# Kernel tuning notes

Hardware: AMD Instinct MI355X
Metric: run time of the kernel (lower is better)

The kernel has to match this reference:

```python
import jax, jax.numpy as jnp
import numpy as np
import math

V, P, D, L, H = 50257, 1024, 768, 12, 12
HD = D // H
DFF = 4 * D
B, S = 2, 1024
EPS = 1e-5


def setup_inputs() -> dict:
    key = jax.random.key(0)
    ks = jax.random.split(key, 8)
    sc = 0.02
    return {
        "input_ids": jax.random.randint(ks[0], (B, S), 0, V),
        "wte": jax.random.normal(ks[1], (V, D), jnp.float32) * sc,
        "wpe": jax.random.normal(ks[2], (P, D), jnp.float32) * sc,
        "ln1_g": jnp.ones((L, D), jnp.float32),
        "ln1_b": jnp.zeros((L, D), jnp.float32),
        "qkv_w": jax.random.normal(ks[3], (L, 3 * D, D), jnp.float32) * sc,
        "qkv_b": jnp.zeros((L, 3 * D), jnp.float32),
        "proj_w": jax.random.normal(ks[4], (L, D, D), jnp.float32) * sc,
        "proj_b": jnp.zeros((L, D), jnp.float32),
        "ln2_g": jnp.ones((L, D), jnp.float32),
        "ln2_b": jnp.zeros((L, D), jnp.float32),
        "fc_w": jax.random.normal(ks[5], (L, DFF, D), jnp.float32) * sc,
        "fc_b": jnp.zeros((L, DFF), jnp.float32),
        "cproj_w": jax.random.normal(ks[6], (L, D, DFF), jnp.float32) * sc,
        "cproj_b": jnp.zeros((L, D), jnp.float32),
        "lnf_g": jnp.ones((D,), jnp.float32),
        "lnf_b": jnp.zeros((D,), jnp.float32),
    }


def layer_norm(x, g, b):
    mu = jnp.mean(x, axis=-1, keepdims=True)
    var = jnp.mean(jnp.square(x - mu), axis=-1, keepdims=True)
    return (x - mu) * jax.lax.rsqrt(var + EPS) * g + b


def _forward(input_ids, wte, wpe, ln1_g, ln1_b, qkv_w, qkv_b, proj_w, proj_b,
             ln2_g, ln2_b, fc_w, fc_b, cproj_w, cproj_b, lnf_g, lnf_b):
    s = input_ids.shape[1]
    h = wte[input_ids] + wpe[jnp.arange(s)][None, :, :]  # [B,S,D]
    causal = jnp.tril(jnp.ones((s, s), bool))  # [S,S]
    neg_inf = jnp.finfo(h.dtype).min

    def step(x, p):
        l1g, l1b, qw, qb, pw, pb, l2g, l2b, fw, fb, cw, cb = p
        hn = layer_norm(x, l1g, l1b)
        qkv = hn @ qw.T + qb  # [B,S,3D]
        q, k, v = jnp.split(qkv, 3, axis=-1)
        q = q.reshape(B, s, H, HD).transpose(0, 2, 1, 3)  # [B,H,S,hd]
        k = k.reshape(B, s, H, HD).transpose(0, 2, 1, 3)
        v = v.reshape(B, s, H, HD).transpose(0, 2, 1, 3)
        scores = jnp.einsum("bhqd,bhkd->bhqk", q, k) / math.sqrt(HD)
        scores = jnp.where(causal[None, None], scores, neg_inf)
        attn = jax.nn.softmax(scores, axis=-1)
        o = jnp.einsum("bhqk,bhkd->bhqd", attn, v)
        o = o.transpose(0, 2, 1, 3).reshape(B, s, D)
        x = x + (o @ pw.T + pb)
        hn2 = layer_norm(x, l2g, l2b)
        m = jax.nn.gelu(hn2 @ fw.T + fb, approximate=False)
        x = x + (m @ cw.T + cb)
        return x, None

    params = (ln1_g, ln1_b, qkv_w, qkv_b, proj_w, proj_b,
              ln2_g, ln2_b, fc_w, fc_b, cproj_w, cproj_b)
    h, _ = jax.lax.scan(step, h, params)
    h = layer_norm(h, lnf_g, lnf_b)
    logits = h @ wte.T  # tied lm_head, [B,S,V]
    return logits


def reference(input_ids, wte, wpe, ln1_g, ln1_b, qkv_w, qkv_b, proj_w, proj_b,
              ln2_g, ln2_b, fc_w, fc_b, cproj_w, cproj_b, lnf_g, lnf_b):
    return _forward(input_ids, wte, wpe, ln1_g, ln1_b, qkv_w, qkv_b, proj_w,
                    proj_b, ln2_g, ln2_b, fc_w, fc_b, cproj_w, cproj_b,
                    lnf_g, lnf_b)
```

## Files before the change

### kernel.cpp

```cpp
#include <hip/hip_runtime.h>

#define BB 2
#define SS 1024
#define DM 768
#define NH 12
#define HDIM 64
#define NL 12
#define DFFN 3072
#define VOC 50257
#define ROWS (BB * SS)
#define MT (ROWS / 128)

typedef __attribute__((ext_vector_type(4))) float f32x4;
typedef __attribute__((ext_vector_type(8))) short short8;
typedef __attribute__((ext_vector_type(4))) short short4v;
typedef unsigned short ushort;

__device__ __forceinline__ ushort f2bf(float f) {
  union { float f; unsigned int u; } x; x.f = f;
  unsigned int u = x.u;
  unsigned int r = (u + 0x7FFFu + ((u >> 16) & 1u)) >> 16;
  return (ushort)r;
}

__global__ __launch_bounds__(256) void embed_k(const int* __restrict__ ids,
    const float* __restrict__ wte, const float* __restrict__ wpe,
    float* __restrict__ h) {
  const int row = blockIdx.x;
  const int s = row & (SS - 1);
  const int tid = threadIdx.x;
  const int id = ids[row];
  const size_t wbase = (size_t)id * DM;
  const size_t pbase = (size_t)s * DM;
  const size_t obase = (size_t)row * DM;
  h[obase + tid]       = wte[wbase + tid]       + wpe[pbase + tid];
  h[obase + tid + 256] = wte[wbase + tid + 256] + wpe[pbase + tid + 256];
  h[obase + tid + 512] = wte[wbase + tid + 512] + wpe[pbase + tid + 512];
}

__global__ __launch_bounds__(256) void f2b_k(const float* __restrict__ in,
                                             ushort* __restrict__ out, int n4) {
  for (int i = blockIdx.x * 256 + threadIdx.x; i < n4; i += gridDim.x * 256) {
    f32x4 v = ((const f32x4*)in)[i];
    short4v s;
    s[0] = f2bf(v[0]); s[1] = f2bf(v[1]); s[2] = f2bf(v[2]); s[3] = f2bf(v[3]);
    ((short4v*)out)[i] = s;
  }
}

template <int OB>
__global__ __launch_bounds__(256) void layernorm_t(const float* __restrict__ x,
    const float* __restrict__ g, const float* __restrict__ b, void* __restrict__ y) {
  const int tid = threadIdx.x;
  const size_t base = (size_t)blockIdx.x * DM;
  float v0 = x[base + tid], v1 = x[base + tid + 256], v2 = x[base + tid + 512];
  __shared__ float red[256];
  red[tid] = v0 + v1 + v2;
  __syncthreads();
  for (int off = 128; off > 0; off >>= 1) {
    if (tid < off) red[tid] += red[tid + off];
    __syncthreads();
  }
  float mu = red[0] * (1.0f / DM);
  __syncthreads();
  float d0 = v0 - mu, d1 = v1 - mu, d2 = v2 - mu;
  red[tid] = d0 * d0 + d1 * d1 + d2 * d2;
  __syncthreads();
  for (int off = 128; off > 0; off >>= 1) {
    if (tid < off) red[tid] += red[tid + off];
    __syncthreads();
  }
  float rstd = rsqrtf(red[0] * (1.0f / DM) + 1e-5f);
  float o0 = d0 * rstd * g[tid]       + b[tid];
  float o1 = d1 * rstd * g[tid + 256] + b[tid + 256];
  float o2 = d2 * rstd * g[tid + 512] + b[tid + 512];
  if (OB) {
    ushort* yo = (ushort*)y;
    yo[base + tid] = f2bf(o0); yo[base + tid + 256] = f2bf(o1);
    yo[base + tid + 512] = f2bf(o2);
  } else {
    float* yo = (float*)y;
    yo[base + tid] = o0; yo[base + tid + 256] = o1; yo[base + tid + 512] = o2;
  }
}

template <int ROUNDS>
__device__ __forceinline__ void stage_sw(const ushort* __restrict__ g, int ldg,
                                         ushort* lds, int wave, int lane,
                                         int rowmax) {
#pragma unroll
  for (int r = 0; r < ROUNDS; r++) {
    const int chunk = (r * 4 + wave) * 64 + lane;
    const int nrow = chunk >> 3;
    const int cs = (chunk & 7) ^ (nrow & 7);
    const int row = nrow > rowmax ? rowmax : nrow;
    const ushort* ga = g + (size_t)row * ldg + cs * 8;
    ushort* la = lds + (r * 4 + wave) * 512;
    __builtin_amdgcn_global_load_lds(
        (const __attribute__((address_space(1))) unsigned int*)ga,
        (__attribute__((address_space(3))) unsigned int*)la, 16, 0, 0);
  }
}

template <int EPI, int OUTBF, int NF>
__global__ __launch_bounds__(256) void gemm_bf(const ushort* __restrict__ A,
    const ushort* __restrict__ Bw, const float* __restrict__ bias,
    const float* __restrict__ res, void* __restrict__ Cout, int N, int K) {
  __shared__ __align__(16) ushort AsL[2][128 * 64];
  __shared__ __align__(16) ushort BsL[2][NF * 32 * 64];
  const int tid = threadIdx.x;
  const int lane = tid & 63;
  const int wave = tid >> 6;
  const int la = lane & 15;
  const int hi = lane >> 4;
  const int swz = (la & 7) << 3;

  const int nwg = gridDim.x;
  int bid = blockIdx.x;
  {
    const int q = nwg >> 3, r = nwg & 7;
    const int xcd = bid & 7, idx = bid >> 3;
    bid = (xcd < r ? xcd * (q + 1) : r * (q + 1) + (xcd - r) * q) + idx;
  }
  const int m0 = (bid % MT) * 128;
  const int n0 = (bid / MT) * (NF * 32);

  const int wr = (wave >> 1) * 64;
  const int wc = (wave & 1) * (NF * 16);
  const int brmax = min(N - n0 - 1, NF * 32 - 1);

  f32x4 acc[4][NF];
#pragma unroll
  for (int i = 0; i < 4; i++)
#pragma unroll
    for (int j = 0; j < NF; j++) acc[i][j] = (f32x4){0.f, 0.f, 0.f, 0.f};

  const ushort* Ag = A + (size_t)m0 * K;
  const ushort* Bg = Bw + (size_t)n0 * K;

  const int nt = K >> 6;
  const int s0 = (bid % MT) % nt;

  stage_sw<4>(Ag + s0 * 64, K, AsL[0], wave, lane, 127);
  stage_sw<NF>(Bg + s0 * 64, K, BsL[0], wave, lane, brmax);

  int cur = 0;
  for (int t = 0; t < nt; t++) {
    if (t + 1 < nt) {
      int sn = t + 1 + s0; if (sn >= nt) sn -= nt;
      stage_sw<4>(Ag + sn * 64, K, AsL[cur ^ 1], wave, lane, 127);
      stage_sw<NF>(Bg + sn * 64, K, BsL[cur ^ 1], wave, lane, brmax);
      asm volatile("s_waitcnt vmcnt(%0)" :: "i"(4 + NF) : "memory");
    } else {
      asm volatile("s_waitcnt vmcnt(0)" ::: "memory");
    }
    __builtin_amdgcn_s_barrier();
    __builtin_amdgcn_sched_barrier(0);

    const ushort* Ab = AsL[cur] + (wr + la) * 64;
    const ushort* Bb = BsL[cur] + (wc + la) * 64;
    __builtin_amdgcn_s_setprio(1);
#pragma unroll
    for (int ks = 0; ks < 2; ks++) {
      const int co = (ks * 32 + hi * 8) ^ swz;
      short8 a[4], b[NF];
#pragma unroll
      for (int mi = 0; mi < 4; mi++)
        a[mi] = *(const short8*)(Ab + mi * 1024 + co);
#pragma unroll
      for (int ni = 0; ni < NF; ni++)
        b[ni] = *(const short8*)(Bb + ni * 1024 + co);
#pragma unroll
      for (int mi = 0; mi < 4; mi++)
#pragma unroll
        for (int ni = 0; ni < NF; ni++)
          acc[mi][ni] = __builtin_amdgcn_mfma_f32_16x16x32_bf16(
              a[mi], b[ni], acc[mi][ni], 0, 0, 0);
    }
    __builtin_amdgcn_s_setprio(0);
    __builtin_amdgcn_sched_barrier(0);
    __builtin_amdgcn_s_barrier();
    __builtin_amdgcn_sched_barrier(0);
    cur ^= 1;
  }

#pragma unroll
  for (int mi = 0; mi < 4; mi++)
#pragma unroll
    for (int ni = 0; ni < NF; ni++) {
      const int col = n0 + wc + ni * 16 + la;
      if (col < N) {
#pragma unroll
        for (int j = 0; j < 4; j++) {
          const int row = m0 + wr + mi * 16 + 4 * hi + j;
          float x = acc[mi][ni][j];
          if (EPI >= 1) x += bias[col];
          const size_t idx = (size_t)row * N + col;
          if (EPI == 2) x += res[idx];
          if (EPI == 3) x = 0.5f * x * (1.0f + erff(x * 0.70710678118f));
          if (OUTBF) ((ushort*)Cout)[idx] = f2bf(x);
          else       ((float*)Cout)[idx] = x;
        }
      }
    }
}

template <int EPI, int OUTBF, int MR>
__global__ __launch_bounds__(256) void gemm_p3(const ushort* __restrict__ A,
    const ushort* __restrict__ Bw, const float* __restrict__ bias,
    const float* __restrict__ res, void* __restrict__ Cout, int N, int K) {
  constexpr int MROWS = MR * 32;
  constexpr int MTILES = ROWS / MROWS;
  constexpr int ASZ = MROWS * 64;
  constexpr int BSZ = 64 * 64;
  __shared__ __align__(16) ushort smem[3 * ASZ + 3 * BSZ];
  ushort* As = smem;
  ushort* Bs = smem + 3 * ASZ;

  const int tid = threadIdx.x;
  const int lane = tid & 63;
  const int wave = tid >> 6;
  const int la = lane & 15;
  const int hi = lane >> 4;
  const int swz = (la & 7) << 3;

  const int nwg = gridDim.x;
  int bid = blockIdx.x;
  {
    const int q = nwg >> 3, r = nwg & 7;
    const int xcd = bid & 7, idx = bid >> 3;
    bid = (xcd < r ? xcd * (q + 1) : r * (q + 1) + (xcd - r) * q) + idx;
  }
  const int m0 = (bid % MTILES) * MROWS;
  const int n0 = (bid / MTILES) * 64;

  const int wr = (wave >> 1) * (MROWS / 2);
  const int wc = (wave & 1) * 32;

  f32x4 acc[MR][2];
#pragma unroll
  for (int i = 0; i < MR; i++)
#pragma unroll
    for (int j = 0; j < 2; j++) acc[i][j] = (f32x4){0.f, 0.f, 0.f, 0.f};

  const ushort* Ag = A + (size_t)m0 * K;
  const ushort* Bg = Bw + (size_t)n0 * K;
  const int nt = K >> 6;
  const int s0 = (bid % MTILES) % nt;

  {
    int s1 = s0 + 1; if (s1 >= nt) s1 -= nt;
    stage_sw<MR>(Ag + s0 * 64, K, As, wave, lane, MROWS - 1);
    stage_sw<2>(Bg + s0 * 64, K, Bs, wave, lane, 63);
    stage_sw<MR>(Ag + s1 * 64, K, As + ASZ, wave, lane, MROWS - 1);
    stage_sw<2>(Bg + s1 * 64, K, Bs + BSZ, wave, lane, 63);
  }

  for (int t = 0; t < nt; t++) {
    if (t + 1 < nt) {
      asm volatile("s_waitcnt vmcnt(%0)" :: "i"(MR + 2) : "memory");
    } else {
      asm volatile("s_waitcnt vmcnt(0)" ::: "memory");
    }
    __builtin_amdgcn_s_barrier();
    __builtin_amdgcn_sched_barrier(0);

    const ushort* Ab = As + (t % 3) * ASZ + (wr + la) * 64;
    const ushort* Bb = Bs + (t % 3) * BSZ + (wc + la) * 64;
    __builtin_amdgcn_s_setprio(1);
#pragma unroll
    for (int ks = 0; ks < 2; ks++) {
      const int co = (ks * 32 + hi * 8) ^ swz;
      short8 a[MR], b[2];
#pragma unroll
      for (int mi = 0; mi < MR; mi++)
        a[mi] = *(const short8*)(Ab + mi * 1024 + co);
#pragma unroll
      for (int ni = 0; ni < 2; ni++)
        b[ni] = *(const short8*)(Bb + ni * 1024 + co);
#pragma unroll
      for (int mi = 0; mi < MR; mi++)
#pragma unroll
        for (int ni = 0; ni < 2; ni++)
          acc[mi][ni] = __builtin_amdgcn_mfma_f32_16x16x32_bf16(
              a[mi], b[ni], acc[mi][ni], 0, 0, 0);
    }
    __builtin_amdgcn_s_setprio(0);
    __builtin_amdgcn_sched_barrier(0);
    __builtin_amdgcn_s_barrier();
    __builtin_amdgcn_sched_barrier(0);
    if (t + 2 < nt) {
      int sn = t + 2 + s0; if (sn >= nt) sn -= nt;
      stage_sw<MR>(Ag + sn * 64, K, As + ((t + 2) % 3) * ASZ, wave, lane, MROWS - 1);
      stage_sw<2>(Bg + sn * 64, K, Bs + ((t + 2) % 3) * BSZ, wave, lane, 63);
    }
  }

  if (OUTBF) {
    ushort* L = smem;
#pragma unroll
    for (int mi = 0; mi < MR; mi++)
#pragma unroll
      for (int ni = 0; ni < 2; ni++)
#pragma unroll
        for (int j = 0; j < 4; j++) {
          const int row = wr + mi * 16 + 4 * hi + j;
          const int col = wc + ni * 16 + la;
          float x = acc[mi][ni][j];
          if (EPI >= 1) x += bias[n0 + col];
          if (EPI == 3) x = 0.5f * x * (1.0f + erff(x * 0.70710678118f));
          L[row * 72 + col] = f2bf(x);
        }
    __syncthreads();
    ushort* Co = (ushort*)Cout;
    constexpr int ITERS = MROWS * 64 / 8 / 256;
#pragma unroll
    for (int it = 0; it < ITERS; it++) {
      const int idx8 = it * 256 + tid;
      const int row = idx8 >> 3, c8 = idx8 & 7;
      short8 v = *(const short8*)&L[row * 72 + c8 * 8];
      *(short8*)&Co[(size_t)(m0 + row) * N + n0 + c8 * 8] = v;
    }
  } else {
    float* L = (float*)smem;
#pragma unroll
    for (int mi = 0; mi < MR; mi++)
#pragma unroll
      for (int ni = 0; ni < 2; ni++)
#pragma unroll
        for (int j = 0; j < 4; j++) {
          const int row = wr + mi * 16 + 4 * hi + j;
          const int col = wc + ni * 16 + la;
          float x = acc[mi][ni][j];
          if (EPI >= 1) x += bias[n0 + col];
          if (EPI == 3) x = 0.5f * x * (1.0f + erff(x * 0.70710678118f));
          L[row * 68 + col] = x;
        }
    __syncthreads();
    f32x4* Co = (f32x4*)Cout;
    const f32x4* R4 = (const f32x4*)res;
    constexpr int ITERS = MROWS * 64 / 4 / 256;
#pragma unroll
    for (int it = 0; it < ITERS; it++) {
      const int idx4 = it * 256 + tid;
      const int row = idx4 >> 4, c4 = idx4 & 15;
      f32x4 v = *(const f32x4*)&L[row * 68 + c4 * 4];
      const size_t o4 = ((size_t)(m0 + row) * N + n0) / 4 + c4;
      if (EPI == 2) v += R4[o4];
      Co[o4] = v;
    }
  }
}

__global__ __launch_bounds__(256) void attn_bf(const ushort* __restrict__ qkv,
                                               ushort* __restrict__ o) {
  const int tid = threadIdx.x;
  const int lane = tid & 63;
  const int wave = tid >> 6;
  const int hi = lane >> 4;
  const int la = lane & 15;
  const int q0 = blockIdx.x * 64;
  const int bh = blockIdx.y;
  const int bb = bh / NH;
  const int hh = bh % NH;
  const size_t rstride = 3 * DM;
  const ushort* base = qkv + (size_t)bb * SS * rstride;

  __shared__ ushort Ks[64][72];
  __shared__ ushort Vt[64][72];
  __shared__ ushort Pb[4][16][72];

  short8 qf[2];
  {
    const int qrow = q0 + wave * 16 + la;
    const ushort* qp = base + (size_t)qrow * rstride + hh * HDIM + 8 * hi;
    qf[0] = *(const short8*)qp;
    qf[1] = *(const short8*)(qp + 32);
  }

  f32x4 accO[4] = {};
  float m_[4], l_[4];
#pragma unroll
  for (int j = 0; j < 4; j++) { m_[j] = -1e30f; l_[j] = 0.f; }

  const int nt = q0 / 64 + 1;
  for (int kt = 0; kt < nt; kt++) {
    __syncthreads();
    {
      const int r = tid >> 2;
      const int c = (tid & 3) * 16;
      const ushort* kp = base + (size_t)(kt * 64 + r) * rstride + DM + hh * HDIM + c;
      const ushort* vp = kp + DM;
      *(short8*)&Ks[r][c]     = *(const short8*)kp;
      *(short8*)&Ks[r][c + 8] = *(const short8*)(kp + 8);
      short8 v0 = *(const short8*)vp;
      short8 v1 = *(const short8*)(vp + 8);
#pragma unroll
      for (int i = 0; i < 8; i++) {
        Vt[c + i][r]     = (ushort)v0[i];
        Vt[c + 8 + i][r] = (ushort)v1[i];
      }
    }
    __syncthreads();

    f32x4 s[4] = {};
#pragma unroll
    for (int f = 0; f < 4; f++) {
#pragma unroll
      for (int kk = 0; kk < 2; kk++) {
        short8 kf = *(const short8*)&Ks[f * 16 + la][kk * 32 + 8 * hi];
        s[f] = __builtin_amdgcn_mfma_f32_16x16x32_bf16(qf[kk], kf, s[f], 0, 0, 0);
      }
#pragma unroll
      for (int j = 0; j < 4; j++) s[f][j] *= 0.125f;
    }

    if (kt == nt - 1) {
      const int qr = wave * 16 + 4 * hi;
#pragma unroll
      for (int f = 0; f < 4; f++) {
        const int kcol = f * 16 + la;
#pragma unroll
        for (int j = 0; j < 4; j++)
          if (kcol > qr + j) s[f][j] = -1e30f;
      }
    }

#pragma unroll
    for (int j = 0; j < 4; j++) {
      float rm = fmaxf(fmaxf(s[0][j], s[1][j]), fmaxf(s[2][j], s[3][j]));
      rm = fmaxf(rm, __shfl_xor(rm, 1));
      rm = fmaxf(rm, __shfl_xor(rm, 2));
      rm = fmaxf(rm, __shfl_xor(rm, 4));
      rm = fmaxf(rm, __shfl_xor(rm, 8));
      const float mnew = fmaxf(m_[j], rm);
      const float alpha = expf(m_[j] - mnew);
      float rs = 0.f;
#pragma unroll
      for (int f = 0; f < 4; f++) {
        const float p = expf(s[f][j] - mnew);
        s[f][j] = p;
        rs += p;
      }
      rs += __shfl_xor(rs, 1);
      rs += __shfl_xor(rs, 2);
      rs += __shfl_xor(rs, 4);
      rs += __shfl_xor(rs, 8);
      l_[j] = l_[j] * alpha + rs;
      m_[j] = mnew;
#pragma unroll
      for (int f = 0; f < 4; f++) accO[f][j] *= alpha;
    }

#pragma unroll
    for (int f = 0; f < 4; f++)
#pragma unroll
      for (int j = 0; j < 4; j++)
        Pb[wave][4 * hi + j][f * 16 + la] = f2bf(s[f][j]);

    short8 pf0 = *(const short8*)&Pb[wave][la][8 * hi];
    short8 pf1 = *(const short8*)&Pb[wave][la][32 + 8 * hi];
#pragma unroll
    for (int f = 0; f < 4; f++) {
      short8 vf0 = *(const short8*)&Vt[f * 16 + la][8 * hi];
      short8 vf1 = *(const short8*)&Vt[f * 16 + la][32 + 8 * hi];
      accO[f] = __builtin_amdgcn_mfma_f32_16x16x32_bf16(pf0, vf0, accO[f], 0, 0, 0);
      accO[f] = __builtin_amdgcn_mfma_f32_16x16x32_bf16(pf1, vf1, accO[f], 0, 0, 0);
    }
  }

  ushort* op = o + (size_t)(bb * SS + q0 + wave * 16) * DM + hh * HDIM;
#pragma unroll
  for (int j = 0; j < 4; j++) {
    const float inv = 1.0f / l_[j];
    const int qr = 4 * hi + j;
#pragma unroll
    for (int f = 0; f < 4; f++)
      op[(size_t)qr * DM + f * 16 + la] = f2bf(accO[f][j] * inv);
  }
}

template <int EPI>
__global__ __launch_bounds__(256) void gemm_nt(const float* __restrict__ A,
    const float* __restrict__ Bw, const float* __restrict__ bias,
    const float* __restrict__ res, float* __restrict__ C, int N, int K) {
  __shared__ ushort As[64][40];
  __shared__ ushort Bs[64][40];
  const int tid = threadIdx.x;
  const int m0 = blockIdx.y * 64;
  const int n0 = blockIdx.x * 64;
  const int lane = tid & 63;
  const int wave = tid >> 6;
  const int wr = (wave >> 1) * 32;
  const int wc = (wave & 1) * 32;
  const int lr = lane & 15;
  const int lk = (lane >> 4) * 8;
  const int sr = tid >> 2;
  const int sc = (tid & 3) * 8;
  f32x4 acc[2][2] = {};
  for (int kk = 0; kk < K; kk += 32) {
    {
      const float* p = A + (size_t)(m0 + sr) * K + kk + sc;
      f32x4 v0 = *(const f32x4*)p;
      f32x4 v1 = *(const f32x4*)(p + 4);
      short8 sv;
      for (int i = 0; i < 4; i++) { sv[i] = f2bf(v0[i]); sv[4 + i] = f2bf(v1[i]); }
      *(short8*)&As[sr][sc] = sv;
    }
    {
      const int gr = n0 + sr;
      short8 sv = {};
      if (gr < N) {
        const float* p = Bw + (size_t)gr * K + kk + sc;
        f32x4 v0 = *(const f32x4*)p;
        f32x4 v1 = *(const f32x4*)(p + 4);
        for (int i = 0; i < 4; i++) { sv[i] = f2bf(v0[i]); sv[4 + i] = f2bf(v1[i]); }
      }
      *(short8*)&Bs[sr][sc] = sv;
    }
    __syncthreads();
    short8 a0 = *(const short8*)&As[wr + lr][lk];
    short8 a1 = *(const short8*)&As[wr + 16 + lr][lk];
    short8 b0 = *(const short8*)&Bs[wc + lr][lk];
    short8 b1 = *(const short8*)&Bs[wc + 16 + lr][lk];
    acc[0][0] = __builtin_amdgcn_mfma_f32_16x16x32_bf16(a0, b0, acc[0][0], 0, 0, 0);
    acc[0][1] = __builtin_amdgcn_mfma_f32_16x16x32_bf16(a0, b1, acc[0][1], 0, 0, 0);
    acc[1][0] = __builtin_amdgcn_mfma_f32_16x16x32_bf16(a1, b0, acc[1][0], 0, 0, 0);
    acc[1][1] = __builtin_amdgcn_mfma_f32_16x16x32_bf16(a1, b1, acc[1][1], 0, 0, 0);
    __syncthreads();
  }
  const int orow = (lane >> 4) * 4;
  for (int mi = 0; mi < 2; mi++)
    for (int ni = 0; ni < 2; ni++) {
      const int col = n0 + wc + ni * 16 + lr;
      if (col >= N) continue;
      for (int j = 0; j < 4; j++) {
        const int row = m0 + wr + mi * 16 + orow + j;
        float x = acc[mi][ni][j];
        if (EPI >= 1) x += bias[col];
        const size_t idx = (size_t)row * N + col;
        if (EPI == 2) x += res[idx];
        if (EPI == 3) x = 0.5f * x * (1.0f + erff(x * 0.70710678118f));
        C[idx] = x;
      }
    }
}

__global__ __launch_bounds__(256) void attn_f32(const float* __restrict__ qkv,
                                                float* __restrict__ o) {
  const int tid = threadIdx.x;
  const int lane = tid & 63;
  const int wave = tid >> 6;
  const int hi = lane >> 4;
  const int la = lane & 15;
  const int q0 = blockIdx.x * 64;
  const int bh = blockIdx.y;
  const int bb = bh / NH;
  const int hh = bh % NH;
  const size_t rstride = 3 * DM;
  const float* base = qkv + (size_t)bb * SS * rstride;
  __shared__ ushort Ks[64][72];
  __shared__ ushort Vt[64][72];
  __shared__ ushort Pb[4][16][72];
  short8 qf[2];
  {
    const int qrow = q0 + wave * 16 + la;
    const float* qp = base + (size_t)qrow * rstride + hh * HDIM + 8 * hi;
    for (int kk = 0; kk < 2; kk++) {
      f32x4 v0 = *(const f32x4*)(qp + 32 * kk);
      f32x4 v1 = *(const f32x4*)(qp + 32 * kk + 4);
      short8 sv;
      for (int i = 0; i < 4; i++) {
        sv[i] = f2bf(v0[i] * 0.125f); sv[4 + i] = f2bf(v1[i] * 0.125f);
      }
      qf[kk] = sv;
    }
  }
  f32x4 accO[4] = {};
  float m_[4], l_[4];
  for (int j = 0; j < 4; j++) { m_[j] = -1e30f; l_[j] = 0.f; }
  const int nt = q0 / 64 + 1;
  for (int kt = 0; kt < nt; kt++) {
    __syncthreads();
    {
      const int r = tid >> 2;
      const int c = (tid & 3) * 16;
      const float* kp = base + (size_t)(kt * 64 + r) * rstride + DM + hh * HDIM + c;
      const float* vp = kp + DM;
      f32x4 k0 = *(const f32x4*)kp, k1 = *(const f32x4*)(kp + 4);
      f32x4 k2 = *(const f32x4*)(kp + 8), k3 = *(const f32x4*)(kp + 12);
      short8 s0, s1;
      for (int i = 0; i < 4; i++) {
        s0[i] = f2bf(k0[i]); s0[4 + i] = f2bf(k1[i]);
        s1[i] = f2bf(k2[i]); s1[4 + i] = f2bf(k3[i]);
      }
      *(short8*)&Ks[r][c] = s0;
      *(short8*)&Ks[r][c + 8] = s1;
      f32x4 v0 = *(const f32x4*)vp, v1 = *(const f32x4*)(vp + 4);
      f32x4 v2 = *(const f32x4*)(vp + 8), v3 = *(const f32x4*)(vp + 12);
      for (int i = 0; i < 4; i++) {
        Vt[c + i][r] = f2bf(v0[i]); Vt[c + 4 + i][r] = f2bf(v1[i]);
        Vt[c + 8 + i][r] = f2bf(v2[i]); Vt[c + 12 + i][r] = f2bf(v3[i]);
      }
    }
    __syncthreads();
    f32x4 s[4] = {};
    for (int f = 0; f < 4; f++)
      for (int kk = 0; kk < 2; kk++) {
        short8 kf = *(const short8*)&Ks[f * 16 + la][kk * 32 + 8 * hi];
        s[f] = __builtin_amdgcn_mfma_f32_16x16x32_bf16(qf[kk], kf, s[f], 0, 0, 0);
      }
    if (kt == nt - 1) {
      const int qr = wave * 16 + 4 * hi;
      for (int f = 0; f < 4; f++) {
        const int kcol = f * 16 + la;
        for (int j = 0; j < 4; j++)
          if (kcol > qr + j) s[f][j] = -1e30f;
      }
    }
    for (int j = 0; j < 4; j++) {
      float rm = fmaxf(fmaxf(s[0][j], s[1][j]), fmaxf(s[2][j], s[3][j]));
      rm = fmaxf(rm, __shfl_xor(rm, 1));
      rm = fmaxf(rm, __shfl_xor(rm, 2));
      rm = fmaxf(rm, __shfl_xor(rm, 4));
      rm = fmaxf(rm, __shfl_xor(rm, 8));
      const float mnew = fmaxf(m_[j], rm);
      const float alpha = expf(m_[j] - mnew);
      float rs = 0.f;
      for (int f = 0; f < 4; f++) {
        const float p = expf(s[f][j] - mnew);
        s[f][j] = p; rs += p;
      }
      rs += __shfl_xor(rs, 1);
      rs += __shfl_xor(rs, 2);
      rs += __shfl_xor(rs, 4);
      rs += __shfl_xor(rs, 8);
      l_[j] = l_[j] * alpha + rs;
      m_[j] = mnew;
      for (int f = 0; f < 4; f++) accO[f][j] *= alpha;
    }
    for (int f = 0; f < 4; f++)
      for (int j = 0; j < 4; j++)
        Pb[wave][4 * hi + j][f * 16 + la] = f2bf(s[f][j]);
    short8 pf0 = *(const short8*)&Pb[wave][la][8 * hi];
    short8 pf1 = *(const short8*)&Pb[wave][la][32 + 8 * hi];
    for (int f = 0; f < 4; f++) {
      short8 vf0 = *(const short8*)&Vt[f * 16 + la][8 * hi];
      short8 vf1 = *(const short8*)&Vt[f * 16 + la][32 + 8 * hi];
      accO[f] = __builtin_amdgcn_mfma_f32_16x16x32_bf16(pf0, vf0, accO[f], 0, 0, 0);
      accO[f] = __builtin_amdgcn_mfma_f32_16x16x32_bf16(pf1, vf1, accO[f], 0, 0, 0);
    }
  }
  float* op = o + (size_t)(bb * SS + q0 + wave * 16) * DM + hh * HDIM;
  for (int j = 0; j < 4; j++) {
    const float inv = 1.0f / l_[j];
    const int qr = 4 * hi + j;
    for (int f = 0; f < 4; f++)
      op[(size_t)qr * DM + f * 16 + la] = accO[f][j] * inv;
  }
}

extern "C" void kernel_launch(void* const* d_in, const int* in_sizes, int n_in,
                              void* d_out, int out_size, void* d_ws,
                              size_t ws_size, hipStream_t stream) {
  const int*   ids     = (const int*)d_in[0];
  const float* wte     = (const float*)d_in[1];
  const float* wpe     = (const float*)d_in[2];
  const float* ln1_g   = (const float*)d_in[3];
  const float* ln1_b   = (const float*)d_in[4];
  const float* qkv_w   = (const float*)d_in[5];
  const float* qkv_b   = (const float*)d_in[6];
  const float* proj_w  = (const float*)d_in[7];
  const float* proj_b  = (const float*)d_in[8];
  const float* ln2_g   = (const float*)d_in[9];
  const float* ln2_b   = (const float*)d_in[10];
  const float* fc_w    = (const float*)d_in[11];
  const float* fc_b    = (const float*)d_in[12];
  const float* cproj_w = (const float*)d_in[13];
  const float* cproj_b = (const float*)d_in[14];
  const float* lnf_g   = (const float*)d_in[15];
  const float* lnf_b   = (const float*)d_in[16];
  float* out = (float*)d_out;

  const size_t sz_h    = (size_t)ROWS * DM * 4;
  const size_t sz_hn   = (size_t)ROWS * DM * 2;
  const size_t sz_qkv  = (size_t)ROWS * 3 * DM * 2;
  const size_t sz_ob   = (size_t)ROWS * DM * 2;
  const size_t sz_mb   = (size_t)ROWS * DFFN * 2;
  const size_t sz_wq   = (size_t)NL * 3 * DM * DM * 2;
  const size_t sz_wp   = (size_t)NL * DM * DM * 2;
  const size_t sz_wf   = (size_t)NL * DFFN * DM * 2;
  const size_t sz_wc   = (size_t)NL * DM * DFFN * 2;
  const size_t sz_wt   = (size_t)VOC * DM * 2;
  const size_t NEED = sz_h + sz_hn + sz_qkv + sz_ob + sz_mb +
                      sz_wq + sz_wp + sz_wf + sz_wc + sz_wt;

  if (ws_size >= NEED) {
    char* p = (char*)d_ws;
    float*  h    = (float*)p;  p += sz_h;
    ushort* hn   = (ushort*)p; p += sz_hn;
    ushort* qkvb = (ushort*)p; p += sz_qkv;
    ushort* ob   = (ushort*)p; p += sz_ob;
    ushort* mb   = (ushort*)p; p += sz_mb;
    ushort* wq   = (ushort*)p; p += sz_wq;
    ushort* wp   = (ushort*)p; p += sz_wp;
    ushort* wf   = (ushort*)p; p += sz_wf;
    ushort* wc   = (ushort*)p; p += sz_wc;
    ushort* wt   = (ushort*)p; p += sz_wt;

    f2b_k<<<2048, 256, 0, stream>>>(qkv_w,   wq, NL * 3 * DM * DM / 4);
    f2b_k<<<1024, 256, 0, stream>>>(proj_w,  wp, NL * DM * DM / 4);
    f2b_k<<<2048, 256, 0, stream>>>(fc_w,    wf, NL * DFFN * DM / 4);
    f2b_k<<<2048, 256, 0, stream>>>(cproj_w, wc, NL * DM * DFFN / 4);
    f2b_k<<<2048, 256, 0, stream>>>(wte,     wt, VOC * DM / 4);

    embed_k<<<ROWS, 256, 0, stream>>>(ids, wte, wpe, h);

    for (int l = 0; l < NL; l++) {
      layernorm_t<1><<<ROWS, 256, 0, stream>>>(h, ln1_g + l * DM, ln1_b + l * DM, hn);
      gemm_p3<1, 1, 4><<<MT * (3 * DM / 64), 256, 0, stream>>>(
          hn, wq + (size_t)l * 3 * DM * DM, qkv_b + (size_t)l * 3 * DM,
          nullptr, qkvb, 3 * DM, DM);
      attn_bf<<<dim3(SS / 64, BB * NH), 256, 0, stream>>>(qkvb, ob);
      gemm_p3<2, 0, 2><<<(ROWS / 64) * (DM / 64), 256, 0, stream>>>(
          ob, wp + (size_t)l * DM * DM, proj_b + (size_t)l * DM, h, h, DM, DM);
      layernorm_t<1><<<ROWS, 256, 0, stream>>>(h, ln2_g + l * DM, ln2_b + l * DM, hn);
      gemm_p3<3, 1, 4><<<MT * (DFFN / 64), 256, 0, stream>>>(
          hn, wf + (size_t)l * DFFN * DM, fc_b + (size_t)l * DFFN,
          nullptr, mb, DFFN, DM);
      gemm_p3<2, 0, 2><<<(ROWS / 64) * (DM / 64), 256, 0, stream>>>(
          mb, wc + (size_t)l * DM * DFFN, cproj_b + (size_t)l * DM, h, h,
          DM, DFFN);
    }

    layernorm_t<1><<<ROWS, 256, 0, stream>>>(h, lnf_g, lnf_b, hn);
    gemm_bf<0, 0, 4><<<MT * ((VOC + 127) / 128), 256, 0, stream>>>(
        hn, wt, nullptr, nullptr, out, VOC, DM);
  } else {
    float* ws = (float*)d_ws;
    float* h   = ws;
    float* hn  = h + (size_t)ROWS * DM;
    float* qkv = hn + (size_t)ROWS * DM;
    float* ob  = qkv + (size_t)ROWS * 3 * DM;
    float* mb  = ob + (size_t)ROWS * DM;

    embed_k<<<ROWS, 256, 0, stream>>>(ids, wte, wpe, h);
    for (int l = 0; l < NL; l++) {
      layernorm_t<0><<<ROWS, 256, 0, stream>>>(h, ln1_g + l * DM, ln1_b + l * DM, hn);
      gemm_nt<1><<<dim3(3 * DM / 64, ROWS / 64), 256, 0, stream>>>(
          hn, qkv_w + (size_t)l * 3 * DM * DM, qkv_b + (size_t)l * 3 * DM,
          nullptr, qkv, 3 * DM, DM);
      attn_f32<<<dim3(SS / 64, BB * NH), 256, 0, stream>>>(qkv, ob);
      gemm_nt<2><<<dim3(DM / 64, ROWS / 64), 256, 0, stream>>>(
          ob, proj_w + (size_t)l * DM * DM, proj_b + (size_t)l * DM, h, h, DM, DM);
      layernorm_t<0><<<ROWS, 256, 0, stream>>>(h, ln2_g + l * DM, ln2_b + l * DM, hn);
      gemm_nt<3><<<dim3(DFFN / 64, ROWS / 64), 256, 0, stream>>>(
          hn, fc_w + (size_t)l * DFFN * DM, fc_b + (size_t)l * DFFN,
          nullptr, mb, DFFN, DM);
      gemm_nt<2><<<dim3(DM / 64, ROWS / 64), 256, 0, stream>>>(
          mb, cproj_w + (size_t)l * DM * DFFN, cproj_b + (size_t)l * DM, h, h,
          DM, DFFN);
    }
    layernorm_t<0><<<ROWS, 256, 0, stream>>>(h, lnf_g, lnf_b, hn);
    gemm_nt<0><<<dim3((VOC + 63) / 64, ROWS / 64), 256, 0, stream>>>(
        hn, wte, nullptr, nullptr, out, VOC, DM);
  }
}
```

Before: 2.073 ms.

## Replace GEMM kernels with 64x64 deep-pipelined tiles and prefetch attention K/V

Swaps the layer GEMMs for a 64x64-tile kernel with a 5-buffer, 4-ahead global-to-LDS prefetch pipeline. The lm_head GEMM now uses 64x128 tiles with triple buffering, replacing the 128x128 double-buffered kernel. The attention kernel now prefetches the next K/V tile into registers while computing the current one, and transposes V with packed 32-bit LDS writes. Smaller tiles give more workgroups and deeper latency hiding, at the cost of less data reuse per tile and more LDS per block.

```diff
diff --git a/kernel.cpp b/kernel.cpp
--- a/kernel.cpp
+++ b/kernel.cpp
@@ -9,7 +9,6 @@
 #define DFFN 3072
 #define VOC 50257
 #define ROWS (BB * SS)
-#define MT (ROWS / 128)
 
 typedef __attribute__((ext_vector_type(4))) float f32x4;
 typedef __attribute__((ext_vector_type(8))) short short8;
@@ -102,12 +101,24 @@
   }
 }
 
-template <int EPI, int OUTBF, int NF>
-__global__ __launch_bounds__(256) void gemm_bf(const ushort* __restrict__ A,
+__device__ __forceinline__ void waitv(int ahead4) {
+  if (ahead4 >= 16)      asm volatile("s_waitcnt vmcnt(16)" ::: "memory");
+  else if (ahead4 == 12) asm volatile("s_waitcnt vmcnt(12)" ::: "memory");
+  else if (ahead4 == 8)  asm volatile("s_waitcnt vmcnt(8)"  ::: "memory");
+  else if (ahead4 == 6)  asm volatile("s_waitcnt vmcnt(6)"  ::: "memory");
+  else if (ahead4 == 4)  asm volatile("s_waitcnt vmcnt(4)"  ::: "memory");
+  else                   asm volatile("s_waitcnt vmcnt(0)"  ::: "memory");
+}
+
+template <int EPI, int OUTBF>
+__global__ __launch_bounds__(256) void gemm_l5(const ushort* __restrict__ A,
     const ushort* __restrict__ Bw, const float* __restrict__ bias,
     const float* __restrict__ res, void* __restrict__ Cout, int N, int K) {
-  __shared__ __align__(16) ushort AsL[2][128 * 64];
-  __shared__ __align__(16) ushort BsL[2][NF * 32 * 64];
+  constexpr int TSZ = 64 * 64;
+  __shared__ __align__(16) ushort smem[10 * TSZ];
+  ushort* As = smem;
+  ushort* Bs = smem + 5 * TSZ;
+
   const int tid = threadIdx.x;
   const int lane = tid & 63;
   const int wave = tid >> 6;
@@ -122,58 +133,62 @@
     const int xcd = bid & 7, idx = bid >> 3;
     bid = (xcd < r ? xcd * (q + 1) : r * (q + 1) + (xcd - r) * q) + idx;
   }
-  const int m0 = (bid % MT) * 128;
-  const int n0 = (bid / MT) * (NF * 32);
-
-  const int wr = (wave >> 1) * 64;
-  const int wc = (wave & 1) * (NF * 16);
-  const int brmax = min(N - n0 - 1, NF * 32 - 1);
-
-  f32x4 acc[4][NF];
-#pragma unroll
-  for (int i = 0; i < 4; i++)
-#pragma unroll
-    for (int j = 0; j < NF; j++) acc[i][j] = (f32x4){0.f, 0.f, 0.f, 0.f};
+  const int m0 = (bid & 31) * 64;
+  const int n0 = (bid >> 5) * 64;
+
+  const int wr = (wave >> 1) * 32;
+  const int wc = (wave & 1) * 32;
+
+  f32x4 acc[2][2];
+#pragma unroll
+  for (int i = 0; i < 2; i++)
+#pragma unroll
+    for (int j = 0; j < 2; j++) acc[i][j] = (f32x4){0.f, 0.f, 0.f, 0.f};
 
   const ushort* Ag = A + (size_t)m0 * K;
   const ushort* Bg = Bw + (size_t)n0 * K;
-
   const int nt = K >> 6;
-  const int s0 = (bid % MT) % nt;
-
-  stage_sw<4>(Ag + s0 * 64, K, AsL[0], wave, lane, 127);
-  stage_sw<NF>(Bg + s0 * 64, K, BsL[0], wave, lane, brmax);
-
-  int cur = 0;
+  const int s0 = (bid & 31) % nt;
+
+#pragma unroll
+  for (int i = 0; i < 4; i++) {
+    if (i < nt) {
+      int sl = s0 + i; if (sl >= nt) sl -= nt;
+      stage_sw<2>(Ag + sl * 64, K, As + i * TSZ, wave, lane, 63);
+      stage_sw<2>(Bg + sl * 64, K, Bs + i * TSZ, wave, lane, 63);
+    }
+  }
+
   for (int t = 0; t < nt; t++) {
-    if (t + 1 < nt) {
-      int sn = t + 1 + s0; if (sn >= nt) sn -= nt;
-      stage_sw<4>(Ag + sn * 64, K, AsL[cur ^ 1], wave, lane, 127);
-      stage_sw<NF>(Bg + sn * 64, K, BsL[cur ^ 1], wave, lane, brmax);
-      asm volatile("s_waitcnt vmcnt(%0)" :: "i"(4 + NF) : "memory");
-    } else {
-      asm volatile("s_waitcnt vmcnt(0)" ::: "memory");
-    }
+    if (t + 4 < nt) {
+      int sl = t + 4 + s0; if (sl >= nt) sl -= nt;
+      const int buf = (t + 4) % 5;
+      stage_sw<2>(Ag + sl * 64, K, As + buf * TSZ, wave, lane, 63);
+      stage_sw<2>(Bg + sl * 64, K, Bs + buf * TSZ, wave, lane, 63);
+    }
+    int ahead = nt - 1 - t; if (ahead > 4) ahead = 4;
+    waitv(ahead * 4);
     __builtin_amdgcn_s_barrier();
     __builtin_amdgcn_sched_barrier(0);
 
-    const ushort* Ab = AsL[cur] + (wr + la) * 64;
-    const ushort* Bb = BsL[cur] + (wc + la) * 64;
+    const int buf = t % 5;
+    const ushort* Ab = As + buf * TSZ + (wr + la) * 64;
+    const ushort* Bb = Bs + buf * TSZ + (wc + la) * 64;
     __builtin_amdgcn_s_setprio(1);
 #pragma unroll
     for (int ks = 0; ks < 2; ks++) {
       const int co = (ks * 32 + hi * 8) ^ swz;
-      short8 a[4], b[NF];
-#pragma unroll
-      for (int mi = 0; mi < 4; mi++)
+      short8 a[2], b[2];
+#pragma unroll
+      for (int mi = 0; mi < 2; mi++)
         a[mi] = *(const short8*)(Ab + mi * 1024 + co);
 #pragma unroll
-      for (int ni = 0; ni < NF; ni++)
+      for (int ni = 0; ni < 2; ni++)
         b[ni] = *(const short8*)(Bb + ni * 1024 + co);
 #pragma unroll
-      for (int mi = 0; mi < 4; mi++)
-#pragma unroll
-        for (int ni = 0; ni < NF; ni++)
+      for (int mi = 0; mi < 2; mi++)
+#pragma unroll
+        for (int ni = 0; ni < 2; ni++)
           acc[mi][ni] = __builtin_amdgcn_mfma_f32_16x16x32_bf16(
               a[mi], b[ni], acc[mi][ni], 0, 0, 0);
     }
@@ -181,125 +196,12 @@
     __builtin_amdgcn_sched_barrier(0);
     __builtin_amdgcn_s_barrier();
     __builtin_amdgcn_sched_barrier(0);
-    cur ^= 1;
-  }
-
-#pragma unroll
-  for (int mi = 0; mi < 4; mi++)
-#pragma unroll
-    for (int ni = 0; ni < NF; ni++) {
-      const int col = n0 + wc + ni * 16 + la;
-      if (col < N) {
-#pragma unroll
-        for (int j = 0; j < 4; j++) {
-          const int row = m0 + wr + mi * 16 + 4 * hi + j;
-          float x = acc[mi][ni][j];
-          if (EPI >= 1) x += bias[col];
-          const size_t idx = (size_t)row * N + col;
-          if (EPI == 2) x += res[idx];
-          if (EPI == 3) x = 0.5f * x * (1.0f + erff(x * 0.70710678118f));
-          if (OUTBF) ((ushort*)Cout)[idx] = f2bf(x);
-          else       ((float*)Cout)[idx] = x;
-        }
-      }
-    }
-}
-
-template <int EPI, int OUTBF, int MR>
-__global__ __launch_bounds__(256) void gemm_p3(const ushort* __restrict__ A,
-    const ushort* __restrict__ Bw, const float* __restrict__ bias,
-    const float* __restrict__ res, void* __restrict__ Cout, int N, int K) {
-  constexpr int MROWS = MR * 32;
-  constexpr int MTILES = ROWS / MROWS;
-  constexpr int ASZ = MROWS * 64;
-  constexpr int BSZ = 64 * 64;
-  __shared__ __align__(16) ushort smem[3 * ASZ + 3 * BSZ];
-  ushort* As = smem;
-  ushort* Bs = smem + 3 * ASZ;
-
-  const int tid = threadIdx.x;
-  const int lane = tid & 63;
-  const int wave = tid >> 6;
-  const int la = lane & 15;
-  const int hi = lane >> 4;
-  const int swz = (la & 7) << 3;
-
-  const int nwg = gridDim.x;
-  int bid = blockIdx.x;
-  {
-    const int q = nwg >> 3, r = nwg & 7;
-    const int xcd = bid & 7, idx = bid >> 3;
-    bid = (xcd < r ? xcd * (q + 1) : r * (q + 1) + (xcd - r) * q) + idx;
-  }
-  const int m0 = (bid % MTILES) * MROWS;
-  const int n0 = (bid / MTILES) * 64;
-
-  const int wr = (wave >> 1) * (MROWS / 2);
-  const int wc = (wave & 1) * 32;
-
-  f32x4 acc[MR][2];
-#pragma unroll
-  for (int i = 0; i < MR; i++)
-#pragma unroll
-    for (int j = 0; j < 2; j++) acc[i][j] = (f32x4){0.f, 0.f, 0.f, 0.f};
-
-  const ushort* Ag = A + (size_t)m0 * K;
-  const ushort* Bg = Bw + (size_t)n0 * K;
-  const int nt = K >> 6;
-  const int s0 = (bid % MTILES) % nt;
-
-  {
-    int s1 = s0 + 1; if (s1 >= nt) s1 -= nt;
-    stage_sw<MR>(Ag + s0 * 64, K, As, wave, lane, MROWS - 1);
-    stage_sw<2>(Bg + s0 * 64, K, Bs, wave, lane, 63);
-    stage_sw<MR>(Ag + s1 * 64, K, As + ASZ, wave, lane, MROWS - 1);
-    stage_sw<2>(Bg + s1 * 64, K, Bs + BSZ, wave, lane, 63);
-  }
-
-  for (int t = 0; t < nt; t++) {
-    if (t + 1 < nt) {
-      asm volatile("s_waitcnt vmcnt(%0)" :: "i"(MR + 2) : "memory");
-    } else {
-      asm volatile("s_waitcnt vmcnt(0)" ::: "memory");
-    }
-    __builtin_amdgcn_s_barrier();
-    __builtin_amdgcn_sched_barrier(0);
-
-    const ushort* Ab = As + (t % 3) * ASZ + (wr + la) * 64;
-    const ushort* Bb = Bs + (t % 3) * BSZ + (wc + la) * 64;
-    __builtin_amdgcn_s_setprio(1);
-#pragma unroll
-    for (int ks = 0; ks < 2; ks++) {
-      const int co = (ks * 32 + hi * 8) ^ swz;
-      short8 a[MR], b[2];
-#pragma unroll
-      for (int mi = 0; mi < MR; mi++)
-        a[mi] = *(const short8*)(Ab + mi * 1024 + co);
-#pragma unroll
-      for (int ni = 0; ni < 2; ni++)
-        b[ni] = *(const short8*)(Bb + ni * 1024 + co);
-#pragma unroll
-      for (int mi = 0; mi < MR; mi++)
-#pragma unroll
-        for (int ni = 0; ni < 2; ni++)
-          acc[mi][ni] = __builtin_amdgcn_mfma_f32_16x16x32_bf16(
-              a[mi], b[ni], acc[mi][ni], 0, 0, 0);
-    }
-    __builtin_amdgcn_s_setprio(0);
-    __builtin_amdgcn_sched_barrier(0);
-    __builtin_amdgcn_s_barrier();
-    __builtin_amdgcn_sched_barrier(0);
-    if (t + 2 < nt) {
-      int sn = t + 2 + s0; if (sn >= nt) sn -= nt;
-      stage_sw<MR>(Ag + sn * 64, K, As + ((t + 2) % 3) * ASZ, wave, lane, MROWS - 1);
-      stage_sw<2>(Bg + sn * 64, K, Bs + ((t + 2) % 3) * BSZ, wave, lane, 63);
-    }
   }
 
   if (OUTBF) {
     ushort* L = smem;
 #pragma unroll
-    for (int mi = 0; mi < MR; mi++)
+    for (int mi = 0; mi < 2; mi++)
 #pragma unroll
       for (int ni = 0; ni < 2; ni++)
 #pragma unroll
@@ -313,9 +215,8 @@
         }
     __syncthreads();
     ushort* Co = (ushort*)Cout;
-    constexpr int ITERS = MROWS * 64 / 8 / 256;
-#pragma unroll
-    for (int it = 0; it < ITERS; it++) {
+#pragma unroll
+    for (int it = 0; it < 2; it++) {
       const int idx8 = it * 256 + tid;
       const int row = idx8 >> 3, c8 = idx8 & 7;
       short8 v = *(const short8*)&L[row * 72 + c8 * 8];
@@ -324,7 +225,7 @@
   } else {
     float* L = (float*)smem;
 #pragma unroll
-    for (int mi = 0; mi < MR; mi++)
+    for (int mi = 0; mi < 2; mi++)
 #pragma unroll
       for (int ni = 0; ni < 2; ni++)
 #pragma unroll
@@ -339,9 +240,8 @@
     __syncthreads();
     f32x4* Co = (f32x4*)Cout;
     const f32x4* R4 = (const f32x4*)res;
-    constexpr int ITERS = MROWS * 64 / 4 / 256;
-#pragma unroll
-    for (int it = 0; it < ITERS; it++) {
+#pragma unroll
+    for (int it = 0; it < 4; it++) {
       const int idx4 = it * 256 + tid;
       const int row = idx4 >> 4, c4 = idx4 & 15;
       f32x4 v = *(const f32x4*)&L[row * 68 + c4 * 4];
@@ -350,6 +250,109 @@
       Co[o4] = v;
     }
   }
+}
+
+__global__ __launch_bounds__(256) void gemm_lg(const ushort* __restrict__ A,
+    const ushort* __restrict__ Bw, float* __restrict__ Cout, int N, int K) {
+  constexpr int ASZ = 64 * 64;
+  constexpr int BSZ = 128 * 64;
+  __shared__ __align__(16) ushort smem[3 * ASZ + 3 * BSZ];
+  ushort* As = smem;
+  ushort* Bs = smem + 3 * ASZ;
+
+  const int tid = threadIdx.x;
+  const int lane = tid & 63;
+  const int wave = tid >> 6;
+  const int la = lane & 15;
+  const int hi = lane >> 4;
+  const int swz = (la & 7) << 3;
+
+  const int nwg = gridDim.x;
+  int bid = blockIdx.x;
+  {
+    const int q = nwg >> 3, r = nwg & 7;
+    const int xcd = bid & 7, idx = bid >> 3;
+    bid = (xcd < r ? xcd * (q + 1) : r * (q + 1) + (xcd - r) * q) + idx;
+  }
+  const int m0 = (bid & 31) * 64;
+  const int n0 = (bid >> 5) * 128;
+
+  const int wr = (wave >> 1) * 32;
+  const int wc = (wave & 1) * 64;
+  const int brmax = min(N - n0 - 1, 127);
+
+  f32x4 acc[2][4];
+#pragma unroll
+  for (int i = 0; i < 2; i++)
+#pragma unroll
+    for (int j = 0; j < 4; j++) acc[i][j] = (f32x4){0.f, 0.f, 0.f, 0.f};
+
+  const ushort* Ag = A + (size_t)m0 * K;
+  const ushort* Bg = Bw + (size_t)n0 * K;
+  const int nt = K >> 6;
+  const int s0 = (bid & 31) % nt;
+
+#pragma unroll
+  for (int i = 0; i < 2; i++) {
+    if (i < nt) {
+      int sl = s0 + i; if (sl >= nt) sl -= nt;
+      stage_sw<2>(Ag + sl * 64, K, As + i * ASZ, wave, lane, 63);
+      stage_sw<4>(Bg + sl * 64, K, Bs + i * BSZ, wave, lane, brmax);
+    }
+  }
+
+  for (int t = 0; t < nt; t++) {
+    if (t + 2 < nt) {
+      int sl = t + 2 + s0; if (sl >= nt) sl -= nt;
+      const int buf = (t + 2) % 3;
+      stage_sw<2>(Ag + sl * 64, K, As + buf * ASZ, wave, lane, 63);
+      stage_sw<4>(Bg + sl * 64, K, Bs + buf * BSZ, wave, lane, brmax);
+    }
+    int ahead = nt - 1 - t; if (ahead > 2) ahead = 2;
+    waitv(ahead * 6);
+    __builtin_amdgcn_s_barrier();
+    __builtin_amdgcn_sched_barrier(0);
+
+    const int buf = t % 3;
+    const ushort* Ab = As + buf * ASZ + (wr + la) * 64;
+    const ushort* Bb = Bs + buf * BSZ + (wc + la) * 64;
+    __builtin_amdgcn_s_setprio(1);
+#pragma unroll
+    for (int ks = 0; ks < 2; ks++) {
+      const int co = (ks * 32 + hi * 8) ^ swz;
+      short8 a[2], b[4];
+#pragma unroll
+      for (int mi = 0; mi < 2; mi++)
+        a[mi] = *(const short8*)(Ab + mi * 1024 + co);
+#pragma unroll
+      for (int ni = 0; ni < 4; ni++)
+        b[ni] = *(const short8*)(Bb + ni * 1024 + co);
+#pragma unroll
+      for (int mi = 0; mi < 2; mi++)
+#pragma unroll
+        for (int ni = 0; ni < 4; ni++)
+          acc[mi][ni] = __builtin_amdgcn_mfma_f32_16x16x32_bf16(
+              a[mi], b[ni], acc[mi][ni], 0, 0, 0);
+    }
+    __builtin_amdgcn_s_setprio(0);
+    __builtin_amdgcn_sched_barrier(0);
+    __builtin_amdgcn_s_barrier();
+    __builtin_amdgcn_sched_barrier(0);
+  }
+
+#pragma unroll
+  for (int mi = 0; mi < 2; mi++)
+#pragma unroll
+    for (int ni = 0; ni < 4; ni++) {
+      const int col = n0 + wc + ni * 16 + la;
+      if (col < N) {
+#pragma unroll
+        for (int j = 0; j < 4; j++) {
+          const int row = m0 + wr + mi * 16 + 4 * hi + j;
+          Cout[(size_t)row * N + col] = acc[mi][ni][j];
+        }
+      }
+    }
 }
 
 __global__ __launch_bounds__(256) void attn_bf(const ushort* __restrict__ qkv,
@@ -365,10 +368,17 @@
   const int hh = bh % NH;
   const size_t rstride = 3 * DM;
   const ushort* base = qkv + (size_t)bb * SS * rstride;
+  const ushort* kbase = base + DM + hh * HDIM;
+  const ushort* vbase = base + 2 * DM + hh * HDIM;
 
   __shared__ ushort Ks[64][72];
   __shared__ ushort Vt[64][72];
   __shared__ ushort Pb[4][16][72];
+
+  const int kr = tid >> 2;
+  const int kc = (tid & 3) * 16;
+  const int vp0 = (tid >> 3) * 2;
+  const int vc = (tid & 7) * 8;
 
   short8 qf[2];
   {
@@ -378,6 +388,16 @@
     qf[1] = *(const short8*)(qp + 32);
   }
 
+  short8 kA, kB, vA, vB;
+  {
+    const ushort* kp = kbase + (size_t)kr * rstride + kc;
+    kA = *(const short8*)kp;
+    kB = *(const short8*)(kp + 8);
+    const ushort* vp = vbase + (size_t)vp0 * rstride + vc;
+    vA = *(const short8*)vp;
+    vB = *(const short8*)(vp + rstride);
+  }
+
   f32x4 accO[4] = {};
   float m_[4], l_[4];
 #pragma unroll
@@ -386,22 +406,23 @@
   const int nt = q0 / 64 + 1;
   for (int kt = 0; kt < nt; kt++) {
     __syncthreads();
-    {
-      const int r = tid >> 2;
-      const int c = (tid & 3) * 16;
-      const ushort* kp = base + (size_t)(kt * 64 + r) * rstride + DM + hh * HDIM + c;
-      const ushort* vp = kp + DM;
-      *(short8*)&Ks[r][c]     = *(const short8*)kp;
-      *(short8*)&Ks[r][c + 8] = *(const short8*)(kp + 8);
-      short8 v0 = *(const short8*)vp;
-      short8 v1 = *(const short8*)(vp + 8);
-#pragma unroll
-      for (int i = 0; i < 8; i++) {
-        Vt[c + i][r]     = (ushort)v0[i];
-        Vt[c + 8 + i][r] = (ushort)v1[i];
-      }
-    }
-    __syncthreads();
+    *(short8*)&Ks[kr][kc]     = kA;
+    *(short8*)&Ks[kr][kc + 8] = kB;
+#pragma unroll
+    for (int i = 0; i < 8; i++) {
+      unsigned int pk = (unsigned int)(unsigned short)vA[i] |
+                        ((unsigned int)(unsigned short)vB[i] << 16);
+      *(unsigned int*)&Vt[vc + i][vp0] = pk;
+    }
+    __syncthreads();
+    if (kt + 1 < nt) {
+      const ushort* kp = kbase + (size_t)((kt + 1) * 64 + kr) * rstride + kc;
+      kA = *(const short8*)kp;
+      kB = *(const short8*)(kp + 8);
+      const ushort* vp = vbase + (size_t)((kt + 1) * 64 + vp0) * rstride + vc;
+      vA = *(const short8*)vp;
+      vB = *(const short8*)(vp + rstride);
+    }
 
     f32x4 s[4] = {};
 #pragma unroll
@@ -718,24 +739,24 @@
 
     for (int l = 0; l < NL; l++) {
       layernorm_t<1><<<ROWS, 256, 0, stream>>>(h, ln1_g + l * DM, ln1_b + l * DM, hn);
-      gemm_p3<1, 1, 4><<<MT * (3 * DM / 64), 256, 0, stream>>>(
+      gemm_l5<1, 1><<<32 * (3 * DM / 64), 256, 0, stream>>>(
           hn, wq + (size_t)l * 3 * DM * DM, qkv_b + (size_t)l * 3 * DM,
           nullptr, qkvb, 3 * DM, DM);
       attn_bf<<<dim3(SS / 64, BB * NH), 256, 0, stream>>>(qkvb, ob);
-      gemm_p3<2, 0, 2><<<(ROWS / 64) * (DM / 64), 256, 0, stream>>>(
+      gemm_l5<2, 0><<<32 * (DM / 64), 256, 0, stream>>>(
           ob, wp + (size_t)l * DM * DM, proj_b + (size_t)l * DM, h, h, DM, DM);
       layernorm_t<1><<<ROWS, 256, 0, stream>>>(h, ln2_g + l * DM, ln2_b + l * DM, hn);
-      gemm_p3<3, 1, 4><<<MT * (DFFN / 64), 256, 0, stream>>>(
+      gemm_l5<3, 1><<<32 * (DFFN / 64), 256, 0, stream>>>(
           hn, wf + (size_t)l * DFFN * DM, fc_b + (size_t)l * DFFN,
           nullptr, mb, DFFN, DM);
-      gemm_p3<2, 0, 2><<<(ROWS / 64) * (DM / 64), 256, 0, stream>>>(
+      gemm_l5<2, 0><<<32 * (DM / 64), 256, 0, stream>>>(
           mb, wc + (size_t)l * DM * DFFN, cproj_b + (size_t)l * DM, h, h,
           DM, DFFN);
     }
 
     layernorm_t<1><<<ROWS, 256, 0, stream>>>(h, lnf_g, lnf_b, hn);
-    gemm_bf<0, 0, 4><<<MT * ((VOC + 127) / 128), 256, 0, stream>>>(
-        hn, wt, nullptr, nullptr, out, VOC, DM);
+    gemm_lg<<<32 * ((VOC + 127) / 128), 256, 0, stream>>>(
+        hn, wt, out, VOC, DM);
   } else {
     float* ws = (float*)d_ws;
     float* h   = ws;
```

New measurement: 2.175 ms. +4.9%, slower.
